# Kernel optimization log

Measured on AMD Instinct MI355X. Metric: run time of the kernel, lower is better.

## Reference

```python
import jax, jax.numpy as jnp
import numpy as np

B, S, H = 1, 2048, 2048
NH, KVH, HD = 32, 8, 64
N_REP = NH // KVH
SCALING = HD ** -0.5
NEG = -1e9  # large negative for causal additive mask


def rotate_half(x):
    x1, x2 = x[..., : HD // 2], x[..., HD // 2:]
    return jnp.concatenate((-x2, x1), axis=-1)


def setup_inputs() -> dict:
    key = jax.random.key(0)
    ks = jax.random.split(key, 6)
    hidden_states = jax.random.normal(ks[0], (B, S, H), dtype=jnp.float32)
    # RoPE tables, Llama style: freqs duplicated across both halves of head_dim
    inv_freq = 1.0 / (10000.0 ** (np.arange(0, HD, 2, dtype=np.float32) / HD))
    t = np.arange(S, dtype=np.float32)
    freqs = np.outer(t, inv_freq)              # [S, HD/2]
    emb = np.concatenate([freqs, freqs], -1)   # [S, HD]
    cos = jnp.asarray(np.cos(emb))[None]       # [1, S, HD]
    sin = jnp.asarray(np.sin(emb))[None]
    # additive causal mask [1,1,S,S]
    causal = jnp.where(jnp.tril(jnp.ones((S, S), bool)), 0.0, NEG).astype(jnp.float32)
    attention_mask = causal[None, None]
    std = 0.02
    Wq = jax.random.normal(ks[1], (NH * HD, H), dtype=jnp.float32) * std
    Wk = jax.random.normal(ks[2], (KVH * HD, H), dtype=jnp.float32) * std
    Wv = jax.random.normal(ks[3], (KVH * HD, H), dtype=jnp.float32) * std
    Wo = jax.random.normal(ks[4], (H, NH * HD), dtype=jnp.float32) * std
    return {"hidden_states": hidden_states, "cos": cos, "sin": sin,
            "attention_mask": attention_mask, "Wq": Wq, "Wk": Wk, "Wv": Wv, "Wo": Wo}


def reference(hidden_states, cos, sin, attention_mask, Wq, Wk, Wv, Wo):
    b, s, _ = hidden_states.shape
    # QKV projections -> [b, heads, s, hd]
    q = (hidden_states @ Wq.T).reshape(b, s, NH, HD).transpose(0, 2, 1, 3)
    k = (hidden_states @ Wk.T).reshape(b, s, KVH, HD).transpose(0, 2, 1, 3)
    v = (hidden_states @ Wv.T).reshape(b, s, KVH, HD).transpose(0, 2, 1, 3)
    # RoPE (cos/sin broadcast over heads via unsqueeze_dim=1)
    c, sn = cos[:, None], sin[:, None]  # [1,1,s,hd]
    q = q * c + rotate_half(q) * sn
    k = k * c + rotate_half(k) * sn
    # GQA repeat_kv (repeat_interleave over head dim)
    k = jnp.repeat(k, N_REP, axis=1)
    v = jnp.repeat(v, N_REP, axis=1)
    # eager attention with explicit [b,h,s,s] score matrix (fp32 softmax)
    scores = jnp.einsum('bhqd,bhkd->bhqk', q, k) * SCALING + attention_mask
    attn_weights = jax.nn.softmax(scores.astype(jnp.float32), axis=-1).astype(q.dtype)
    attn = jnp.einsum('bhqk,bhkd->bhqd', attn_weights, v)
    attn = attn.transpose(0, 2, 1, 3).reshape(b, s, NH * HD)
    out = attn @ Wo.T
    return out, attn_weights
```

## Files before the change

### kernel.cpp

```cpp
#include <hip/hip_runtime.h>
#include <hip/hip_bf16.h>
#include <type_traits>

#define S_LEN 2048
#define HDIM  2048
#define NHEADS 32
#define KVHEADS 8
#define HD 64
#define SCALE 0.125f

typedef __bf16 bf16;
typedef bf16  bf16x8 __attribute__((ext_vector_type(8)));
typedef float f32x4  __attribute__((ext_vector_type(4)));
typedef unsigned int u32;

__device__ __forceinline__ void gload16(const void* g, void* l) {
  __builtin_amdgcn_global_load_lds((const __attribute__((address_space(1))) void*)g,
                                   (__attribute__((address_space(3))) void*)l, 16, 0, 0);
}

template<int RB>
__device__ __forceinline__ bf16x8 frag_ld(const bf16* lds, int row, int kByte, int lane) {
  const char* p = reinterpret_cast<const char*>(lds) + row*RB
                + ((kByte + ((lane>>4)<<4)) ^ ((row&7)<<4));
  return *reinterpret_cast<const bf16x8*>(p);
}

__device__ __forceinline__ f32x4 mfma16(bf16x8 a, bf16x8 b, f32x4 c) {
  return __builtin_amdgcn_mfma_f32_16x16x32_bf16(a, b, c, 0, 0, 0);
}

__global__ void cvt_all(const float* __restrict__ hs, const float* __restrict__ wq,
                        const float* __restrict__ wk, const float* __restrict__ wv,
                        const float* __restrict__ wo, bf16* __restrict__ dst) {
  size_t c = (size_t)blockIdx.x*256 + threadIdx.x;
  const float* src;
  if      (c <  524288u)  src = hs + c*8;
  else if (c < 1048576u)  src = wq + (c - 524288u)*8;
  else if (c < 1179648u)  src = wk + (c - 1048576u)*8;
  else if (c < 1310720u)  src = wv + (c - 1179648u)*8;
  else                    src = wo + (c - 1310720u)*8;
  float4 a = *reinterpret_cast<const float4*>(src);
  float4 b = *reinterpret_cast<const float4*>(src + 4);
  bf16x8 o;
  o[0]=(bf16)a.x; o[1]=(bf16)a.y; o[2]=(bf16)a.z; o[3]=(bf16)a.w;
  o[4]=(bf16)b.x; o[5]=(bf16)b.y; o[6]=(bf16)b.z; o[7]=(bf16)b.w;
  *reinterpret_cast<bf16x8*>(dst + c*8) = o;
}

enum { EPI_QKV = 0, EPI_OUT = 2 };

template<int EPI>
__global__ __launch_bounds__(256, 3) void gemm_bt(
    const bf16* __restrict__ A, const bf16* __restrict__ Bw,
    void* __restrict__ C0, void* __restrict__ C1, void* __restrict__ C2,
    const float* __restrict__ cosp, const float* __restrict__ sinp,
    int N, int K)
{
  __shared__ __align__(16) bf16 lsA[2][128*64];
  __shared__ __align__(16) bf16 lsB[2][64*64];
  const int t = threadIdx.x, lane = t & 63;
  const int w = t >> 6;
  const int bm = blockIdx.x, bn = blockIdx.y;
  const int r8 = t >> 3, c8 = t & 7;
  const int llo = lane & 15, lhi = lane >> 4;
  const int nkt = K >> 6;

  auto stage = [&](int kt, int b) {
    #pragma unroll
    for (int i = 0; i < 4; i++) {
      int row = i*32 + r8;
      int chunk = c8 ^ (row & 7);
      gload16(A + (size_t)(bm*128 + row)*K + kt*64 + chunk*8,
              (char*)(&lsA[b][0]) + i*4096 + t*16);
    }
    #pragma unroll
    for (int i = 0; i < 2; i++) {
      int row = i*32 + r8;
      int chunk = c8 ^ (row & 7);
      gload16(Bw + (size_t)(bn*64 + row)*K + kt*64 + chunk*8,
              (char*)(&lsB[b][0]) + i*4096 + t*16);
    }
  };

  f32x4 acc[2][4] = {};
  stage(0, 0);
  for (int kt = 0; kt < nkt; ++kt) {
    if (kt + 1 < nkt) {
      stage(kt + 1, (kt + 1) & 1);
      asm volatile("s_waitcnt vmcnt(6)" ::: "memory");
    } else {
      asm volatile("s_waitcnt vmcnt(0)" ::: "memory");
    }
    __builtin_amdgcn_s_barrier();
    asm volatile("" ::: "memory");
    const bf16* lA = &lsA[kt & 1][0];
    const bf16* lB = &lsB[kt & 1][0];
    #pragma unroll
    for (int ks = 0; ks < 2; ++ks) {
      bf16x8 av[2], bv[4];
      #pragma unroll
      for (int m = 0; m < 2; m++) av[m] = frag_ld<128>(lA, w*32 + m*16 + llo, ks*64, lane);
      #pragma unroll
      for (int n = 0; n < 4; n++) bv[n] = frag_ld<128>(lB, n*16 + llo, ks*64, lane);
      #pragma unroll
      for (int m = 0; m < 2; m++)
        #pragma unroll
        for (int n = 0; n < 4; n++)
          acc[m][n] = mfma16(av[m], bv[n], acc[m][n]);
    }
    asm volatile("s_waitcnt lgkmcnt(0)" ::: "memory");
    __builtin_amdgcn_s_barrier();
    asm volatile("" ::: "memory");
  }

  const int rowb = bm*128 + w*32 + lhi*4;
  const int colb = bn*64;
  if constexpr (EPI == EPI_OUT) {
    float* C = (float*)C0;
    #pragma unroll
    for (int m = 0; m < 2; m++)
      #pragma unroll
      for (int n = 0; n < 4; n++)
        #pragma unroll
        for (int r = 0; r < 4; r++) {
          int row = rowb + m*16 + r;
          int col = colb + n*16 + llo;
          __builtin_nontemporal_store(acc[m][n][r], &C[(size_t)row*HDIM + col]);
        }
  } else {
    if (bn < 40) {
      #pragma unroll
      for (int m = 0; m < 2; m++)
        #pragma unroll
        for (int r = 0; r < 4; r++) {
          int row = rowb + m*16 + r;
          #pragma unroll
          for (int n = 0; n < 4; n++) {
            int d = n*16 + llo;
            float v  = acc[m][n][r];
            float pr = acc[m][n^2][r];
            float rot = (n & 2) ? pr : -pr;
            float cv = cosp[(size_t)row*HD + d];
            float sv = sinp[(size_t)row*HD + d];
            float o = v*cv + rot*sv;
            if (bn < 32) {
              ((bf16*)C0)[((size_t)bn*S_LEN + row)*HD + d] = (bf16)(o*SCALE);
            } else {
              ((bf16*)C1)[((size_t)(bn-32)*S_LEN + row)*HD + d] = (bf16)o;
            }
          }
        }
    } else {
      bf16* lsT = &lsA[0][0];
      #pragma unroll
      for (int m = 0; m < 2; m++)
        #pragma unroll
        for (int n = 0; n < 4; n++)
          #pragma unroll
          for (int r = 0; r < 4; r++) {
            int d  = n*16 + llo;
            int sl = w*32 + m*16 + lhi*4 + r;
            char* pp = (char*)lsT + d*256 + ((sl*2) ^ ((d & 7) << 4));
            *(bf16*)pp = (bf16)acc[m][n][r];
          }
      __syncthreads();
      bf16* vT = (bf16*)C2;
      #pragma unroll
      for (int i = 0; i < 4; i++) {
        int rid = i*16 + (t >> 4);
        int c   = t & 15;
        bf16x8 v = *(const bf16x8*)((char*)lsT + rid*256 + ((c*16) ^ ((rid & 7) << 4)));
        *reinterpret_cast<bf16x8*>(
          vT + ((size_t)(bn-40)*HD + rid)*S_LEN + bm*128 + c*8) = v;
      }
    }
  }
}

__global__ __launch_bounds__(256, 2) void attn_kernel(
    const bf16* __restrict__ qB, const bf16* __restrict__ kB, const bf16* __restrict__ vTB,
    float* __restrict__ attnw, bf16* __restrict__ aB)
{
  __shared__ __align__(16) bf16 lsP[128*128];
  __shared__ float lstat[256];
  const int t = threadIdx.x, lane = t & 63;
  const int w = t >> 6, wm = w & 1, wn = w >> 1;
  const int b = blockIdx.x;
  const int h = b >> 4;
  const int qraw = b & 15;
  const int qt = (b < 256) ? qraw : 15 - qraw;
  const int kvh = h >> 2;
  const int llo = lane & 15, lhi = lane >> 4;

  bf16x8 qa[4][2];
  #pragma unroll
  for (int m = 0; m < 4; m++)
    #pragma unroll
    for (int ks = 0; ks < 2; ks++)
      qa[m][ks] = *reinterpret_cast<const bf16x8*>(
        qB + ((size_t)h*S_LEN + qt*128 + wm*64 + m*16 + llo)*HD + ks*32 + lhi*8);

  float l_r[4][4];
  #pragma unroll
  for (int m = 0; m < 4; m++)
    #pragma unroll
    for (int r = 0; r < 4; r++) l_r[m][r] = 0.f;

  auto tileA = [&](int kt, auto diag_c) {
    constexpr bool DIAG = decltype(diag_c)::value;
    bf16x8 kb[4][2];
    #pragma unroll
    for (int n = 0; n < 4; n++)
      #pragma unroll
      for (int ks = 0; ks < 2; ks++)
        kb[n][ks] = *reinterpret_cast<const bf16x8*>(
          kB + ((size_t)kvh*S_LEN + kt*128 + wn*64 + n*16 + llo)*HD + ks*32 + lhi*8);
    f32x4 accs[4][4] = {};
    __builtin_amdgcn_s_setprio(1);
    #pragma unroll
    for (int ks = 0; ks < 2; ++ks)
      #pragma unroll
      for (int m = 0; m < 4; m++)
        #pragma unroll
        for (int n = 0; n < 4; n++) {
          if (DIAG && (wn*64 + n*16 > wm*64 + m*16 + 15)) continue;
          accs[m][n] = mfma16(qa[m][ks], kb[n][ks], accs[m][n]);
        }
    __builtin_amdgcn_s_setprio(0);
    #pragma unroll
    for (int m = 0; m < 4; m++) {
      #pragma unroll
      for (int r = 0; r < 4; r++) {
        if constexpr (DIAG) {
          int grow = qt*128 + wm*64 + m*16 + lhi*4 + r;
          #pragma unroll
          for (int n = 0; n < 4; n++) {
            int gcol = kt*128 + wn*64 + n*16 + llo;
            l_r[m][r] += (gcol > grow) ? 0.f : __expf(accs[m][n][r]);
          }
        } else {
          #pragma unroll
          for (int n = 0; n < 4; n++) l_r[m][r] += __expf(accs[m][n][r]);
        }
      }
    }
  };
  for (int kt = 0; kt < qt; ++kt) tileA(kt, std::false_type{});
  tileA(qt, std::true_type{});

  #pragma unroll
  for (int m = 0; m < 4; m++)
    #pragma unroll
    for (int r = 0; r < 4; r++) {
      float se = l_r[m][r];
      #pragma unroll
      for (int off = 1; off < 16; off <<= 1) se += __shfl_xor(se, off);
      l_r[m][r] = se;
    }
  if (llo == 0) {
    #pragma unroll
    for (int m = 0; m < 4; m++)
      #pragma unroll
      for (int r = 0; r < 4; r++)
        lstat[wn*128 + wm*64 + m*16 + lhi*4 + r] = l_r[m][r];
  }
  __syncthreads();
  float linv[4][4];
  #pragma unroll
  for (int m = 0; m < 4; m++)
    #pragma unroll
    for (int r = 0; r < 4; r++) {
      int rg = wm*64 + m*16 + lhi*4 + r;
      linv[m][r] = 1.0f / (lstat[rg] + lstat[128 + rg]);
    }

  f32x4 acco[4][2] = {};
  float* awb = attnw + (size_t)h*S_LEN*S_LEN;

  auto tileB = [&](int kt, auto diag_c) {
    constexpr bool DIAG = decltype(diag_c)::value;
    bf16x8 kb[4][2];
    #pragma unroll
    for (int n = 0; n < 4; n++)
      #pragma unroll
      for (int ks = 0; ks < 2; ks++)
        kb[n][ks] = *reinterpret_cast<const bf16x8*>(
          kB + ((size_t)kvh*S_LEN + kt*128 + wn*64 + n*16 + llo)*HD + ks*32 + lhi*8);
    bf16x8 vb[2][4];
    #pragma unroll
    for (int n = 0; n < 2; n++)
      #pragma unroll
      for (int ks = 0; ks < 4; ks++)
        vb[n][ks] = *reinterpret_cast<const bf16x8*>(
          vTB + ((size_t)kvh*HD + wn*32 + n*16 + llo)*S_LEN + kt*128 + ks*32 + lhi*8);
    f32x4 accs[4][4] = {};
    __builtin_amdgcn_s_setprio(1);
    #pragma unroll
    for (int ks = 0; ks < 2; ++ks)
      #pragma unroll
      for (int m = 0; m < 4; m++)
        #pragma unroll
        for (int n = 0; n < 4; n++) {
          if (DIAG && (wn*64 + n*16 > wm*64 + m*16 + 15)) continue;
          accs[m][n] = mfma16(qa[m][ks], kb[n][ks], accs[m][n]);
        }
    __builtin_amdgcn_s_setprio(0);
    #pragma unroll
    for (int m = 0; m < 4; m++) {
      #pragma unroll
      for (int r = 0; r < 4; r++) {
        int rl = wm*64 + m*16 + lhi*4 + r;
        int grow = qt*128 + rl;
        float li = linv[m][r];
        #pragma unroll
        for (int n = 0; n < 4; n++) {
          int cl = wn*64 + n*16 + llo;
          int gcol = kt*128 + cl;
          float p;
          if constexpr (DIAG) {
            p = (gcol > grow) ? 0.f : __expf(accs[m][n][r])*li;
            if (gcol <= grow)
              __builtin_nontemporal_store(p, &awb[(size_t)grow*S_LEN + gcol]);
          } else {
            p = __expf(accs[m][n][r])*li;
            __builtin_nontemporal_store(p, &awb[(size_t)grow*S_LEN + gcol]);
          }
          char* pp = (char*)lsP + rl*256 + ((cl*2) ^ ((rl & 7) << 4));
          *(bf16*)pp = (bf16)p;
        }
      }
    }
    asm volatile("s_waitcnt lgkmcnt(0)" ::: "memory");
    __builtin_amdgcn_s_barrier();
    asm volatile("" ::: "memory");
    __builtin_amdgcn_s_setprio(1);
    #pragma unroll
    for (int ks = 0; ks < 4; ++ks) {
      bf16x8 pa[4];
      #pragma unroll
      for (int m = 0; m < 4; m++) pa[m] = frag_ld<256>(lsP, wm*64 + m*16 + llo, ks*64, lane);
      #pragma unroll
      for (int m = 0; m < 4; m++)
        #pragma unroll
        for (int n = 0; n < 2; n++)
          acco[m][n] = mfma16(pa[m], vb[n][ks], acco[m][n]);
    }
    __builtin_amdgcn_s_setprio(0);
    asm volatile("s_waitcnt lgkmcnt(0)" ::: "memory");
    __builtin_amdgcn_s_barrier();
    asm volatile("" ::: "memory");
  };
  for (int kt = 0; kt < qt; ++kt) tileB(kt, std::false_type{});
  tileB(qt, std::true_type{});

  #pragma unroll
  for (int m = 0; m < 4; m++)
    #pragma unroll
    for (int n = 0; n < 2; n++)
      #pragma unroll
      for (int r = 0; r < 4; r++) {
        int rl = wm*64 + m*16 + lhi*4 + r;
        int cl = wn*32 + n*16 + llo;
        char* pp = (char*)lsP + rl*128 + ((cl*2) ^ ((rl & 7) << 4));
        *(bf16*)pp = (bf16)acco[m][n][r];
      }
  __syncthreads();
  #pragma unroll
  for (int i = 0; i < 4; i++) {
    int rl = i*32 + (t >> 3);
    int c  = t & 7;
    bf16x8 v = *(const bf16x8*)((char*)lsP + rl*128 + ((c*16) ^ ((rl & 7) << 4)));
    *reinterpret_cast<bf16x8*>(aB + (size_t)(qt*128 + rl)*HDIM + h*HD + c*8) = v;
  }
}

extern "C" void kernel_launch(void* const* d_in, const int* in_sizes, int n_in,
                              void* d_out, int out_size, void* d_ws, size_t ws_size,
                              hipStream_t stream)
{
  (void)in_sizes; (void)n_in; (void)out_size; (void)ws_size;
  const float* hs   = (const float*)d_in[0];
  const float* cosp = (const float*)d_in[1];
  const float* sinp = (const float*)d_in[2];
  const float* Wq   = (const float*)d_in[4];
  const float* Wk   = (const float*)d_in[5];
  const float* Wv   = (const float*)d_in[6];
  const float* Wo   = (const float*)d_in[7];

  const size_t M4 = 4u*1024*1024, M1 = 1024u*1024;
  bf16* hsB = (bf16*)d_ws;
  bf16* WqB = hsB + M4;
  bf16* WkB = WqB + M4;
  bf16* WvB = WkB + M1;
  bf16* WoB = WvB + M1;
  bf16* qB  = WoB + M4;
  bf16* kB  = qB  + M4;
  bf16* vTB = kB  + M1;
  bf16* aB  = vTB + M1;

  float* outp  = (float*)d_out;
  float* attnw = outp + (size_t)S_LEN*HDIM;

  cvt_all<<<7168, 256, 0, stream>>>(hs, Wq, Wk, Wv, Wo, hsB);

  gemm_bt<EPI_QKV><<<dim3(16,48), 256, 0, stream>>>(hsB, WqB, qB, kB, vTB, cosp, sinp, 3072, 2048);
  attn_kernel<<<512, 256, 0, stream>>>(qB, kB, vTB, attnw, aB);
  gemm_bt<EPI_OUT><<<dim3(16,32), 256, 0, stream>>>(aB, WoB, outp, nullptr, nullptr,
                                                    nullptr, nullptr, 2048, 2048);
}
```

Before: 212.2 us.

## Halve attention query tile to 64 rows and double-buffer P tile in LDS

The attention kernel now processes 64 query rows per block instead of 128, doubling the grid to 1024 blocks and raising launch bounds to 4 blocks per CU. The P staging buffer is double-buffered by key-tile parity, which removes the trailing barrier after each PV step. The aim is better load balance and occupancy for the causal workload, at the cost of reloading K/V tiles twice as often per query row. Each key tile is still 128 wide, so the diagonal tile masks more wasted work.

```diff
diff --git a/kernel.cpp b/kernel.cpp
--- a/kernel.cpp
+++ b/kernel.cpp
@@ -178,34 +178,32 @@
   }
 }
 
-__global__ __launch_bounds__(256, 2) void attn_kernel(
+__global__ __launch_bounds__(256, 4) void attn_kernel(
     const bf16* __restrict__ qB, const bf16* __restrict__ kB, const bf16* __restrict__ vTB,
     float* __restrict__ attnw, bf16* __restrict__ aB)
 {
-  __shared__ __align__(16) bf16 lsP[128*128];
-  __shared__ float lstat[256];
+  __shared__ __align__(16) bf16 lsP[2][64*128];
+  __shared__ float lstat[128];
   const int t = threadIdx.x, lane = t & 63;
   const int w = t >> 6, wm = w & 1, wn = w >> 1;
   const int b = blockIdx.x;
-  const int h = b >> 4;
-  const int qraw = b & 15;
-  const int qt = (b < 256) ? qraw : 15 - qraw;
+  const int h = b >> 5;
+  const int qraw = b & 31;
+  const int qt = (b < 512) ? qraw : 31 - qraw;
+  const int q0 = qt*64;
+  const int ktmax = qt >> 1;
   const int kvh = h >> 2;
   const int llo = lane & 15, lhi = lane >> 4;
 
-  bf16x8 qa[4][2];
+  bf16x8 qa[2][2];
   #pragma unroll
-  for (int m = 0; m < 4; m++)
+  for (int m = 0; m < 2; m++)
     #pragma unroll
     for (int ks = 0; ks < 2; ks++)
       qa[m][ks] = *reinterpret_cast<const bf16x8*>(
-        qB + ((size_t)h*S_LEN + qt*128 + wm*64 + m*16 + llo)*HD + ks*32 + lhi*8);
-
-  float l_r[4][4];
-  #pragma unroll
-  for (int m = 0; m < 4; m++)
-    #pragma unroll
-    for (int r = 0; r < 4; r++) l_r[m][r] = 0.f;
+        qB + ((size_t)h*S_LEN + q0 + wm*32 + m*16 + llo)*HD + ks*32 + lhi*8);
+
+  float l_r[2][4] = {};
 
   auto tileA = [&](int kt, auto diag_c) {
     constexpr bool DIAG = decltype(diag_c)::value;
@@ -216,24 +214,24 @@
       for (int ks = 0; ks < 2; ks++)
         kb[n][ks] = *reinterpret_cast<const bf16x8*>(
           kB + ((size_t)kvh*S_LEN + kt*128 + wn*64 + n*16 + llo)*HD + ks*32 + lhi*8);
-    f32x4 accs[4][4] = {};
+    f32x4 accs[2][4] = {};
     __builtin_amdgcn_s_setprio(1);
     #pragma unroll
     for (int ks = 0; ks < 2; ++ks)
       #pragma unroll
-      for (int m = 0; m < 4; m++)
+      for (int m = 0; m < 2; m++)
         #pragma unroll
         for (int n = 0; n < 4; n++) {
-          if (DIAG && (wn*64 + n*16 > wm*64 + m*16 + 15)) continue;
+          if (DIAG && (kt*128 + wn*64 + n*16 > q0 + wm*32 + m*16 + 15)) continue;
           accs[m][n] = mfma16(qa[m][ks], kb[n][ks], accs[m][n]);
         }
     __builtin_amdgcn_s_setprio(0);
     #pragma unroll
-    for (int m = 0; m < 4; m++) {
+    for (int m = 0; m < 2; m++)
       #pragma unroll
       for (int r = 0; r < 4; r++) {
         if constexpr (DIAG) {
-          int grow = qt*128 + wm*64 + m*16 + lhi*4 + r;
+          int grow = q0 + wm*32 + m*16 + lhi*4 + r;
           #pragma unroll
           for (int n = 0; n < 4; n++) {
             int gcol = kt*128 + wn*64 + n*16 + llo;
@@ -244,13 +242,12 @@
           for (int n = 0; n < 4; n++) l_r[m][r] += __expf(accs[m][n][r]);
         }
       }
-    }
   };
-  for (int kt = 0; kt < qt; ++kt) tileA(kt, std::false_type{});
-  tileA(qt, std::true_type{});
+  for (int kt = 0; kt < ktmax; ++kt) tileA(kt, std::false_type{});
+  tileA(ktmax, std::true_type{});
 
   #pragma unroll
-  for (int m = 0; m < 4; m++)
+  for (int m = 0; m < 2; m++)
     #pragma unroll
     for (int r = 0; r < 4; r++) {
       float se = l_r[m][r];
@@ -260,26 +257,27 @@
     }
   if (llo == 0) {
     #pragma unroll
-    for (int m = 0; m < 4; m++)
+    for (int m = 0; m < 2; m++)
       #pragma unroll
       for (int r = 0; r < 4; r++)
-        lstat[wn*128 + wm*64 + m*16 + lhi*4 + r] = l_r[m][r];
+        lstat[wn*64 + wm*32 + m*16 + lhi*4 + r] = l_r[m][r];
   }
   __syncthreads();
-  float linv[4][4];
+  float linv[2][4];
   #pragma unroll
-  for (int m = 0; m < 4; m++)
+  for (int m = 0; m < 2; m++)
     #pragma unroll
     for (int r = 0; r < 4; r++) {
-      int rg = wm*64 + m*16 + lhi*4 + r;
-      linv[m][r] = 1.0f / (lstat[rg] + lstat[128 + rg]);
-    }
-
-  f32x4 acco[4][2] = {};
+      int rg = wm*32 + m*16 + lhi*4 + r;
+      linv[m][r] = 1.0f / (lstat[rg] + lstat[64 + rg]);
+    }
+
+  f32x4 acco[2][2] = {};
   float* awb = attnw + (size_t)h*S_LEN*S_LEN;
 
   auto tileB = [&](int kt, auto diag_c) {
     constexpr bool DIAG = decltype(diag_c)::value;
+    bf16* lp = &lsP[kt & 1][0];
     bf16x8 kb[4][2];
     #pragma unroll
     for (int n = 0; n < 4; n++)
@@ -294,24 +292,24 @@
       for (int ks = 0; ks < 4; ks++)
         vb[n][ks] = *reinterpret_cast<const bf16x8*>(
           vTB + ((size_t)kvh*HD + wn*32 + n*16 + llo)*S_LEN + kt*128 + ks*32 + lhi*8);
-    f32x4 accs[4][4] = {};
+    f32x4 accs[2][4] = {};
     __builtin_amdgcn_s_setprio(1);
     #pragma unroll
     for (int ks = 0; ks < 2; ++ks)
       #pragma unroll
-      for (int m = 0; m < 4; m++)
+      for (int m = 0; m < 2; m++)
         #pragma unroll
         for (int n = 0; n < 4; n++) {
-          if (DIAG && (wn*64 + n*16 > wm*64 + m*16 + 15)) continue;
+          if (DIAG && (kt*128 + wn*64 + n*16 > q0 + wm*32 + m*16 + 15)) continue;
           accs[m][n] = mfma16(qa[m][ks], kb[n][ks], accs[m][n]);
         }
     __builtin_amdgcn_s_setprio(0);
     #pragma unroll
-    for (int m = 0; m < 4; m++) {
+    for (int m = 0; m < 2; m++)
       #pragma unroll
       for (int r = 0; r < 4; r++) {
-        int rl = wm*64 + m*16 + lhi*4 + r;
-        int grow = qt*128 + rl;
+        int rl = wm*32 + m*16 + lhi*4 + r;
+        int grow = q0 + rl;
         float li = linv[m][r];
         #pragma unroll
         for (int n = 0; n < 4; n++) {
@@ -326,52 +324,49 @@
             p = __expf(accs[m][n][r])*li;
             __builtin_nontemporal_store(p, &awb[(size_t)grow*S_LEN + gcol]);
           }
-          char* pp = (char*)lsP + rl*256 + ((cl*2) ^ ((rl & 7) << 4));
+          char* pp = (char*)lp + rl*256 + ((cl*2) ^ ((rl & 7) << 4));
           *(bf16*)pp = (bf16)p;
         }
       }
-    }
     asm volatile("s_waitcnt lgkmcnt(0)" ::: "memory");
     __builtin_amdgcn_s_barrier();
     asm volatile("" ::: "memory");
     __builtin_amdgcn_s_setprio(1);
     #pragma unroll
     for (int ks = 0; ks < 4; ++ks) {
-      bf16x8 pa[4];
-      #pragma unroll
-      for (int m = 0; m < 4; m++) pa[m] = frag_ld<256>(lsP, wm*64 + m*16 + llo, ks*64, lane);
-      #pragma unroll
-      for (int m = 0; m < 4; m++)
+      bf16x8 pa[2];
+      #pragma unroll
+      for (int m = 0; m < 2; m++) pa[m] = frag_ld<256>(lp, wm*32 + m*16 + llo, ks*64, lane);
+      #pragma unroll
+      for (int m = 0; m < 2; m++)
         #pragma unroll
         for (int n = 0; n < 2; n++)
           acco[m][n] = mfma16(pa[m], vb[n][ks], acco[m][n]);
     }
     __builtin_amdgcn_s_setprio(0);
-    asm volatile("s_waitcnt lgkmcnt(0)" ::: "memory");
-    __builtin_amdgcn_s_barrier();
-    asm volatile("" ::: "memory");
   };
-  for (int kt = 0; kt < qt; ++kt) tileB(kt, std::false_type{});
-  tileB(qt, std::true_type{});
-
+  for (int kt = 0; kt < ktmax; ++kt) tileB(kt, std::false_type{});
+  tileB(ktmax, std::true_type{});
+
+  __syncthreads();
   #pragma unroll
-  for (int m = 0; m < 4; m++)
+  for (int m = 0; m < 2; m++)
     #pragma unroll
     for (int n = 0; n < 2; n++)
       #pragma unroll
       for (int r = 0; r < 4; r++) {
-        int rl = wm*64 + m*16 + lhi*4 + r;
+        int rl = wm*32 + m*16 + lhi*4 + r;
         int cl = wn*32 + n*16 + llo;
-        char* pp = (char*)lsP + rl*128 + ((cl*2) ^ ((rl & 7) << 4));
+        char* pp = (char*)&lsP[0][0] + rl*128 + ((cl*2) ^ ((rl & 7) << 4));
         *(bf16*)pp = (bf16)acco[m][n][r];
       }
   __syncthreads();
   #pragma unroll
-  for (int i = 0; i < 4; i++) {
+  for (int i = 0; i < 2; i++) {
     int rl = i*32 + (t >> 3);
     int c  = t & 7;
-    bf16x8 v = *(const bf16x8*)((char*)lsP + rl*128 + ((c*16) ^ ((rl & 7) << 4)));
-    *reinterpret_cast<bf16x8*>(aB + (size_t)(qt*128 + rl)*HDIM + h*HD + c*8) = v;
+    bf16x8 v = *(const bf16x8*)((char*)&lsP[0][0] + rl*128 + ((c*16) ^ ((rl & 7) << 4)));
+    *reinterpret_cast<bf16x8*>(aB + (size_t)(q0 + rl)*HDIM + h*HD + c*8) = v;
   }
 }
 
@@ -405,7 +400,7 @@
   cvt_all<<<7168, 256, 0, stream>>>(hs, Wq, Wk, Wv, Wo, hsB);
 
   gemm_bt<EPI_QKV><<<dim3(16,48), 256, 0, stream>>>(hsB, WqB, qB, kB, vTB, cosp, sinp, 3072, 2048);
-  attn_kernel<<<512, 256, 0, stream>>>(qB, kB, vTB, attnw, aB);
+  attn_kernel<<<1024, 256, 0, stream>>>(qB, kB, vTB, attnw, aB);
   gemm_bt<EPI_OUT><<<dim3(16,32), 256, 0, stream>>>(aB, WoB, outp, nullptr, nullptr,
                                                     nullptr, nullptr, 2048, 2048);
 }
```

Result: slower. 316.3 us (+49.0%).
